# Optimization experiments

Measured on AMD Instinct MI355X. Metric: run time of the kernel, lower is better.

Reference implementation:

```python
import jax, jax.numpy as jnp
import numpy as np

B, T, DC, DS, H, V = 8, 1024, 128, 128, 512, 50000
LENGTHS = np.array([2, 4])  # dictionary word lengths for slot 0 and slot 1
LMAX = 4                    # ring-buffer size >= max word length


def setup_inputs() -> dict:
    key = jax.random.key(0)
    ks = jax.random.split(key, 12)
    s = 0.05
    return {
        "char_emb": jax.random.normal(ks[0], (B, T, DC), jnp.float32),
        "word_ids": jax.random.randint(ks[1], (B, T, 2), 0, V),
        "sense_table": jax.random.normal(ks[2], (V, DS), jnp.float32),
        "w_ih": jax.random.normal(ks[3], (DC, 3 * H), jnp.float32) * s,
        "w_hh": jax.random.normal(ks[4], (H, 3 * H), jnp.float32) * s,
        "b": jnp.zeros((3 * H,), jnp.float32),
        "aw_ih": jax.random.normal(ks[5], (DC, H), jnp.float32) * s,
        "aw_hh": jax.random.normal(ks[6], (H, H), jnp.float32) * s,
        "ab": jnp.zeros((H,), jnp.float32),
        "ww_ih": jax.random.normal(ks[7], (DS, 3 * H), jnp.float32) * s,
        "ww_hh": jax.random.normal(ks[8], (H, 3 * H), jnp.float32) * s,
        "wb": jnp.zeros((3 * H,), jnp.float32),
    }


def _forward(char_emb, word_ids, sense_table, w_ih, w_hh, b,
             aw_ih, aw_hh, ab, ww_ih, ww_hh, wb):
    H_ = w_hh.shape[0]
    T_ = char_emb.shape[1]
    lengths = jnp.asarray(LENGTHS)
    slot_idx = jnp.arange(2)

    def run_seq(x_seq, wid_seq):
        # pend: ring buffer of pending word-cell states [LMAX, 2, H]
        def step(carry, t):
            h, c, pend, pmask = carry
            x = x_seq[t]
            # --- MultiInputLSTMCell (char cell) ---
            gates = x @ w_ih + h @ w_hh + b              # [3H]
            i = jax.nn.sigmoid(gates[:H_])
            o = jax.nn.sigmoid(gates[H_:2 * H_])
            g = jnp.tanh(gates[2 * H_:])
            r = jnp.mod(t, LMAX)
            cins = pend[r]                                # [2, H] incoming word cells
            m = pmask[r].astype(x.dtype)                  # [2] validity
            alpha = jax.nn.sigmoid(x @ aw_ih + ab + cins @ aw_hh)  # [2, H]
            ea = jnp.exp(alpha) * m[:, None]
            ei = jnp.exp(i)
            denom = ei + ea.sum(0)
            c_lat = (ei * g + (ea * cins).sum(0)) / denom
            c_plain = (1.0 - i) * c + i * g               # c_num == 0 path: f = 1 - i
            c1 = jnp.where(pmask[r].any(), c_lat, c_plain)
            h1 = o * jnp.tanh(c1)
            # consume the ring slot for this timestep
            pend = pend.at[r].set(0.0)
            pmask = pmask.at[r].set(False)
            # --- WordLSTMCell for words starting at t ---
            xw = sense_table[wid_seq[t]]                  # [2, DS]
            wg = xw @ ww_ih + h1 @ ww_hh + wb             # [2, 3H]
            f = jax.nn.sigmoid(wg[:, :H_])
            iw = jax.nn.sigmoid(wg[:, H_:2 * H_])
            gw = jnp.tanh(wg[:, 2 * H_:])
            cw = f * c1 + iw * gw                         # [2, H]
            ends = t + lengths - 1
            valid = ends < T_
            wslots = jnp.mod(ends, LMAX)
            old = pend[wslots, slot_idx]
            pend = pend.at[wslots, slot_idx].set(jnp.where(valid[:, None], cw, old))
            pmask = pmask.at[wslots, slot_idx].set(valid | pmask[wslots, slot_idx])
            return (h1, c1, pend, pmask), (h1, c1)

        carry0 = (jnp.zeros((H_,), x_seq.dtype), jnp.zeros((H_,), x_seq.dtype),
                  jnp.zeros((LMAX, 2, H_), x_seq.dtype), jnp.zeros((LMAX, 2), bool))
        _, (hs, cs) = jax.lax.scan(step, carry0, jnp.arange(T_))
        return hs, cs

    hs, cs = jax.vmap(run_seq)(char_emb, word_ids)
    return jnp.stack((hs, cs))  # [2, B, T, H]


def reference(char_emb, word_ids, sense_table, w_ih, w_hh, b,
              aw_ih, aw_hh, ab, ww_ih, ww_hh, wb):
    return _forward(char_emb, word_ids, sense_table, w_ih, w_hh, b,
                    aw_ih, aw_hh, ab, ww_ih, ww_hh, wb)
```

## Files before the change

### kernel.cpp

```cpp
#include <hip/hip_runtime.h>
#include <hip/hip_bf16.h>


#define Bq 8
#define Tq 1024
#define DCq 128
#define Hq 512
#define NWG 32
#define NTHR 256

typedef unsigned long long u64;

#define HPUB_OFF  0u
#define PENDP_OFF 65536u
#define WIHT_OFF  327680u
#define WHHT_OFF  720896u
#define AWIHT_OFF 2293760u
#define AWHHT_OFF 2424832u
#define WWIHT_OFF 2949120u
#define WWHHT_OFF 3342336u

__device__ __forceinline__ float bflo(unsigned u){ return __uint_as_float(u << 16); }
__device__ __forceinline__ float bfhi(unsigned u){ return __uint_as_float(u & 0xffff0000u); }
__device__ __forceinline__ float sigm(float x){ return 1.0f / (1.0f + __expf(-x)); }

__device__ __forceinline__ void fma4(float& acc, uint2 w, float4 v){
  acc = fmaf(bflo(w.x), v.x, acc);
  acc = fmaf(bfhi(w.x), v.y, acc);
  acc = fmaf(bflo(w.y), v.z, acc);
  acc = fmaf(bfhi(w.y), v.w, acc);
}

__device__ __forceinline__ float red16(float x){
  x += __shfl_xor(x, 8, 16);
  x += __shfl_xor(x, 4, 16);
  x += __shfl_xor(x, 2, 16);
  x += __shfl_xor(x, 1, 16);
  return x;
}

__device__ __forceinline__ u64 pack64(float v, unsigned gen){
  return ((u64)gen << 32) | (u64)__float_as_uint(v);
}
__device__ __forceinline__ void pub64(u64* p, float v, unsigned gen){
  __hip_atomic_store(p, pack64(v, gen), __ATOMIC_RELAXED, __HIP_MEMORY_SCOPE_AGENT);
}
__device__ __forceinline__ u64 ld64(const u64* p){
  return __hip_atomic_load(p, __ATOMIC_RELAXED, __HIP_MEMORY_SCOPE_AGENT);
}
__device__ __forceinline__ unsigned genof(u64 v){ return (unsigned)(v >> 32); }
__device__ __forceinline__ float valof(u64 v){ return __uint_as_float((unsigned)v); }

__global__ void transpose_bf16(const float* __restrict__ src, __hip_bfloat16* __restrict__ dst,
                               int kshift, int total, int N){
  const int K = 1 << kshift;
  for (int idx = blockIdx.x * blockDim.x + threadIdx.x; idx < total;
       idx += gridDim.x * blockDim.x){
    int n = idx >> kshift;
    int k = idx & (K - 1);
    dst[idx] = __float2bfloat16(src[(size_t)k * N + n]);
  }
}

__global__ void __launch_bounds__(NTHR, 1)
lattice_main(const float* __restrict__ char_emb,
             const int*   __restrict__ word_ids,
             const float* __restrict__ sense_table,
             const float* __restrict__ bias_b,
             const float* __restrict__ bias_ab,
             const float* __restrict__ bias_wb,
             unsigned char* __restrict__ ws,
             float* __restrict__ out)
{
  const int seq  = blockIdx.x;
  const int wg   = blockIdx.y;
  const int tid  = threadIdx.x;
  const int grp  = tid >> 4;
  const int lane = tid & 15;
  const int J    = wg * 16 + grp;
  const int i0   = tid * 2, i1 = tid * 2 + 1;

  u64* hpub = (u64*)(ws + HPUB_OFF)  + (size_t)seq * 2 * Hq;
  u64* pnd  = (u64*)(ws + PENDP_OFF) + (size_t)seq * 4 * 2 * Hq;

  const uint2* w_ihT  = (const uint2*)(ws + WIHT_OFF);
  const uint2* w_hhT  = (const uint2*)(ws + WHHT_OFF);
  const uint2* aw_ihT = (const uint2*)(ws + AWIHT_OFF);
  const uint2* aw_hhT = (const uint2*)(ws + AWHHT_OFF);
  const uint2* ww_ihT = (const uint2*)(ws + WWIHT_OFF);
  const uint2* ww_hhT = (const uint2*)(ws + WWHHT_OFF);

  uint2 Rwhh_i[8], Rwhh_o[8], Rwhh_g[8], Rawhh[8];
  uint2 Rwwh_f[8], Rwwh_i[8], Rwwh_g[8];
  uint2 Rwih_i[2], Rwih_o[2], Rwih_g[2], Rawih[2];
  uint2 Rwwi_f[2], Rwwi_i[2], Rwwi_g[2];
  {
    const uint2* whh_i = w_hhT  + (size_t)(0*Hq + J) * 128;
    const uint2* whh_o = w_hhT  + (size_t)(1*Hq + J) * 128;
    const uint2* whh_g = w_hhT  + (size_t)(2*Hq + J) * 128;
    const uint2* awhh  = aw_hhT + (size_t)J * 128;
    const uint2* wwh_f = ww_hhT + (size_t)(0*Hq + J) * 128;
    const uint2* wwh_i = ww_hhT + (size_t)(1*Hq + J) * 128;
    const uint2* wwh_g = ww_hhT + (size_t)(2*Hq + J) * 128;
#pragma unroll
    for (int it = 0; it < 8; ++it){
      const int q = it * 16 + lane;
      Rwhh_i[it] = whh_i[q];  Rwhh_o[it] = whh_o[q];  Rwhh_g[it] = whh_g[q];
      Rawhh[it]  = awhh[q];
      Rwwh_f[it] = wwh_f[q];  Rwwh_i[it] = wwh_i[q];  Rwwh_g[it] = wwh_g[q];
    }
    const uint2* wih_i = w_ihT  + (size_t)(0*Hq + J) * 32;
    const uint2* wih_o = w_ihT  + (size_t)(1*Hq + J) * 32;
    const uint2* wih_g = w_ihT  + (size_t)(2*Hq + J) * 32;
    const uint2* awih  = aw_ihT + (size_t)J * 32;
    const uint2* wwi_f = ww_ihT + (size_t)(0*Hq + J) * 32;
    const uint2* wwi_i = ww_ihT + (size_t)(1*Hq + J) * 32;
    const uint2* wwi_g = ww_ihT + (size_t)(2*Hq + J) * 32;
#pragma unroll
    for (int it = 0; it < 2; ++it){
      const int q = it * 16 + lane;
      Rwih_i[it] = wih_i[q];  Rwih_o[it] = wih_o[q];  Rwih_g[it] = wih_g[q];
      Rawih[it]  = awih[q];
      Rwwi_f[it] = wwi_f[q];  Rwwi_i[it] = wwi_i[q];  Rwwi_g[it] = wwi_g[q];
    }
  }

  const float b_i  = bias_b[J], b_o = bias_b[Hq + J], b_g = bias_b[2*Hq + J];
  const float ab_J = bias_ab[J];
  const float wb_f = bias_wb[J], wb_i = bias_wb[Hq + J], wb_g = bias_wb[2*Hq + J];

  float* out_h = out + (size_t)seq * Tq * Hq;
  float* out_c = out + ((size_t)Bq + seq) * Tq * Hq;

  __shared__ __align__(16) float shH[2][Hq];
  __shared__ __align__(16) float sh_p0[Hq];
  __shared__ __align__(16) float sh_p1[Hq];
  __shared__ __align__(16) float shx[2][DCq];
  __shared__ __align__(16) float shxw0[2][DCq];
  __shared__ __align__(16) float shxw1[2][DCq];

  shH[0][i0] = 0.f; shH[0][i1] = 0.f;
  shH[1][i0] = 0.f; shH[1][i1] = 0.f;
  sh_p0[i0] = 0.f; sh_p0[i1] = 0.f;
  sh_p1[i0] = 0.f; sh_p1[i1] = 0.f;
  if (tid < DCq){
    shx[0][tid] = char_emb[((size_t)seq * Tq + 0) * DCq + tid];
  } else {
    const int k = tid - DCq;
    const int w0 = word_ids[(size_t)seq * Tq * 2 + 0];
    const int w1 = word_ids[(size_t)seq * Tq * 2 + 1];
    shxw0[0][k] = sense_table[(size_t)w0 * DCq + k];
    shxw1[0][k] = sense_table[(size_t)w1 * DCq + k];
  }
  __syncthreads();

  for (int t = 0; t < Tq; ++t){
    const int par = t & 1;
    const float* hprev = shH[par ^ 1];

    float a_i = 0.f, a_o = 0.f, a_g = 0.f, a_xa = 0.f;
#pragma unroll
    for (int it = 0; it < 8; ++it){
      const int k0 = it * 64 + lane * 4;
      float4 hv = *(const float4*)(hprev + k0);
      fma4(a_i, Rwhh_i[it], hv);
      fma4(a_o, Rwhh_o[it], hv);
      fma4(a_g, Rwhh_g[it], hv);
    }
#pragma unroll
    for (int it = 0; it < 2; ++it){
      const int k0 = it * 64 + lane * 4;
      float4 xv = *(const float4*)(shx[par] + k0);
      fma4(a_i,  Rwih_i[it], xv);
      fma4(a_o,  Rwih_o[it], xv);
      fma4(a_g,  Rwih_g[it], xv);
      fma4(a_xa, Rawih[it],  xv);
    }

    if (t >= 3){
      const u64* p0 = pnd + ((size_t)(t & 3) * 2 + 0) * Hq;
      const u64* p1 = pnd + ((size_t)(t & 3) * 2 + 1) * Hq;
      const unsigned tg0 = (unsigned)t, tg1 = (unsigned)(t - 2);
      u64 a, b, c, d;
      for (;;){
        a = ld64(p0 + i0); b = ld64(p0 + i1);
        c = ld64(p1 + i0); d = ld64(p1 + i1);
        if (genof(a) >= tg0 && genof(b) >= tg0 &&
            genof(c) >= tg1 && genof(d) >= tg1) break;
      }
      sh_p0[i0] = valof(a); sh_p0[i1] = valof(b);
      sh_p1[i0] = valof(c); sh_p1[i1] = valof(d);
    } else if (t >= 1){
      const u64* p0 = pnd + ((size_t)(t & 3) * 2 + 0) * Hq;
      const unsigned tg0 = (unsigned)t;
      u64 a, b;
      for (;;){
        a = ld64(p0 + i0); b = ld64(p0 + i1);
        if (genof(a) >= tg0 && genof(b) >= tg0) break;
      }
      sh_p0[i0] = valof(a); sh_p0[i1] = valof(b);
    }
    __syncthreads();

    float a_p0 = 0.f, a_p1 = 0.f;
#pragma unroll
    for (int it = 0; it < 8; ++it){
      const int k0 = it * 64 + lane * 4;
      float4 p0v = *(const float4*)(sh_p0 + k0);
      float4 p1v = *(const float4*)(sh_p1 + k0);
      fma4(a_p0, Rawhh[it], p0v);
      fma4(a_p1, Rawhh[it], p1v);
    }
    a_i  = red16(a_i);  a_o  = red16(a_o);  a_g  = red16(a_g);
    a_xa = red16(a_xa); a_p0 = red16(a_p0); a_p1 = red16(a_p1);

    const float gi = sigm(a_i + b_i);
    const float go = sigm(a_o + b_o);
    const float gg = tanhf(a_g + b_g);
    float c1;
    if (t == 0){
      c1 = gi * gg;
    } else {
      const float base = a_xa + ab_J;
      const float ea0 = __expf(sigm(base + a_p0));
      const float ei  = __expf(gi);
      float num = ei * gg + ea0 * sh_p0[J];
      float den = ei + ea0;
      if (t >= 3){
        const float ea1 = __expf(sigm(base + a_p1));
        num += ea1 * sh_p1[J];
        den += ea1;
      }
      c1 = num / den;
    }
    const float h1 = go * tanhf(c1);
    if (lane == 0){
      pub64(hpub + (size_t)par * Hq + J, h1, (unsigned)(t + 1));
      out_h[(size_t)t * Hq + J] = h1;
      out_c[(size_t)t * Hq + J] = c1;
    }

    {
      const int tn = (t + 1 < Tq) ? t + 1 : t;
      if (tid < DCq){
        shx[par ^ 1][tid] = char_emb[((size_t)seq * Tq + tn) * DCq + tid];
      } else {
        const int k = tid - DCq;
        const int w0 = word_ids[((size_t)seq * Tq + tn) * 2 + 0];
        const int w1 = word_ids[((size_t)seq * Tq + tn) * 2 + 1];
        shxw0[par ^ 1][k] = sense_table[(size_t)w0 * DCq + k];
        shxw1[par ^ 1][k] = sense_table[(size_t)w1 * DCq + k];
      }
      const u64* hp = hpub + (size_t)par * Hq;
      const unsigned tg = (unsigned)(t + 1);
      u64 a, b;
      for (;;){
        a = ld64(hp + i0); b = ld64(hp + i1);
        if (genof(a) >= tg && genof(b) >= tg) break;
      }
      shH[par][i0] = valof(a); shH[par][i1] = valof(b);
    }
    __syncthreads();

    float r_f = 0.f, r_i = 0.f, r_g = 0.f;
    float x_f0 = 0.f, x_i0 = 0.f, x_g0 = 0.f, x_f1 = 0.f, x_i1 = 0.f, x_g1 = 0.f;
#pragma unroll
    for (int it = 0; it < 8; ++it){
      const int k0 = it * 64 + lane * 4;
      float4 hv = *(const float4*)(shH[par] + k0);
      fma4(r_f, Rwwh_f[it], hv);
      fma4(r_i, Rwwh_i[it], hv);
      fma4(r_g, Rwwh_g[it], hv);
    }
#pragma unroll
    for (int it = 0; it < 2; ++it){
      const int k0 = it * 64 + lane * 4;
      float4 x0 = *(const float4*)(shxw0[par] + k0);
      float4 x1 = *(const float4*)(shxw1[par] + k0);
      fma4(x_f0, Rwwi_f[it], x0);  fma4(x_f1, Rwwi_f[it], x1);
      fma4(x_i0, Rwwi_i[it], x0);  fma4(x_i1, Rwwi_i[it], x1);
      fma4(x_g0, Rwwi_g[it], x0);  fma4(x_g1, Rwwi_g[it], x1);
    }
    r_f  = red16(r_f);  r_i  = red16(r_i);  r_g  = red16(r_g);
    x_f0 = red16(x_f0); x_i0 = red16(x_i0); x_g0 = red16(x_g0);
    x_f1 = red16(x_f1); x_i1 = red16(x_i1); x_g1 = red16(x_g1);

    if (lane == 0){
      const float f0  = sigm(r_f + x_f0 + wb_f);
      const float iw0 = sigm(r_i + x_i0 + wb_i);
      const float g0  = tanhf(r_g + x_g0 + wb_g);
      const float cw0 = f0 * c1 + iw0 * g0;
      const float f1  = sigm(r_f + x_f1 + wb_f);
      const float iw1 = sigm(r_i + x_i1 + wb_i);
      const float g1  = tanhf(r_g + x_g1 + wb_g);
      const float cw1 = f1 * c1 + iw1 * g1;
      pub64(pnd + ((size_t)((t + 1) & 3) * 2 + 0) * Hq + J, cw0, (unsigned)(t + 1));
      pub64(pnd + ((size_t)((t + 3) & 3) * 2 + 1) * Hq + J, cw1, (unsigned)(t + 1));
    }
  }
}

extern "C" void kernel_launch(void* const* d_in, const int* in_sizes, int n_in,
                              void* d_out, int out_size, void* d_ws, size_t ws_size,
                              hipStream_t stream){
  const float* char_emb = (const float*)d_in[0];
  const int*   word_ids = (const int*)d_in[1];
  const float* sense    = (const float*)d_in[2];
  const float* w_ih     = (const float*)d_in[3];
  const float* w_hh     = (const float*)d_in[4];
  const float* bb       = (const float*)d_in[5];
  const float* aw_ih    = (const float*)d_in[6];
  const float* aw_hh    = (const float*)d_in[7];
  const float* ab       = (const float*)d_in[8];
  const float* ww_ih    = (const float*)d_in[9];
  const float* ww_hh    = (const float*)d_in[10];
  const float* wb       = (const float*)d_in[11];
  unsigned char* ws = (unsigned char*)d_ws;
  float* out = (float*)d_out;

  hipMemsetAsync(ws, 0, WIHT_OFF, stream);

  transpose_bf16<<<512, NTHR, 0, stream>>>(w_ih,  (__hip_bfloat16*)(ws + WIHT_OFF),  7, 128*1536, 1536);
  transpose_bf16<<<512, NTHR, 0, stream>>>(w_hh,  (__hip_bfloat16*)(ws + WHHT_OFF),  9, 512*1536, 1536);
  transpose_bf16<<<512, NTHR, 0, stream>>>(aw_ih, (__hip_bfloat16*)(ws + AWIHT_OFF), 7, 128*512,  512);
  transpose_bf16<<<512, NTHR, 0, stream>>>(aw_hh, (__hip_bfloat16*)(ws + AWHHT_OFF), 9, 512*512,  512);
  transpose_bf16<<<512, NTHR, 0, stream>>>(ww_ih, (__hip_bfloat16*)(ws + WWIHT_OFF), 7, 128*1536, 1536);
  transpose_bf16<<<512, NTHR, 0, stream>>>(ww_hh, (__hip_bfloat16*)(ws + WWHHT_OFF), 9, 512*1536, 1536);

  dim3 grid(Bq, NWG);
  lattice_main<<<grid, NTHR, 0, stream>>>(char_emb, word_ids, sense, bb, ab, wb, ws, out);
}
```

Measured before the change: 5.606 ms.

## Add XCD-local fast sync path with sc0 loads and hoist word-input matvec

At startup, each workgroup reads its XCC id and publishes it, and the sequence's workgroups check whether all of them landed on the same XCD. If they did, cross-workgroup h and pending-cell exchanges use sc0-scoped global loads and stores into a separate fast buffer, falling back to the agent-scope buffer after a bounded spin. The intent is to cut the latency of the per-step cross-WG handoff by staying within the local L2 instead of going through device coherence. It also moves the word-input matvec ahead of the h spin-wait so that work overlaps the wait. The risks are extra dual stores every step and no benefit if workgroups are spread across XCDs, which is likely for the default blockIdx mapping.

```diff
diff --git a/kernel.cpp b/kernel.cpp
--- a/kernel.cpp
+++ b/kernel.cpp
@@ -8,17 +8,21 @@
 #define Hq 512
 #define NWG 32
 #define NTHR 256
+#define SPINF 64
 
 typedef unsigned long long u64;
 
-#define HPUB_OFF  0u
-#define PENDP_OFF 65536u
-#define WIHT_OFF  327680u
-#define WHHT_OFF  720896u
-#define AWIHT_OFF 2293760u
-#define AWHHT_OFF 2424832u
-#define WWIHT_OFF 2949120u
-#define WWHHT_OFF 3342336u
+#define HPUBF_OFF 0u
+#define PENDF_OFF 65536u
+#define HPUBS_OFF 327680u
+#define PENDS_OFF 393216u
+#define XCD_OFF   655360u
+#define WIHT_OFF  657408u
+#define WHHT_OFF  1050624u
+#define AWIHT_OFF 2623488u
+#define AWHHT_OFF 2754560u
+#define WWIHT_OFF 3278848u
+#define WWHHT_OFF 3672064u
 
 __device__ __forceinline__ float bflo(unsigned u){ return __uint_as_float(u << 16); }
 __device__ __forceinline__ float bfhi(unsigned u){ return __uint_as_float(u & 0xffff0000u); }
@@ -42,14 +46,38 @@
 __device__ __forceinline__ u64 pack64(float v, unsigned gen){
   return ((u64)gen << 32) | (u64)__float_as_uint(v);
 }
-__device__ __forceinline__ void pub64(u64* p, float v, unsigned gen){
-  __hip_atomic_store(p, pack64(v, gen), __ATOMIC_RELAXED, __HIP_MEMORY_SCOPE_AGENT);
+__device__ __forceinline__ void pub64(u64* p, u64 v){
+  __hip_atomic_store(p, v, __ATOMIC_RELAXED, __HIP_MEMORY_SCOPE_AGENT);
 }
 __device__ __forceinline__ u64 ld64(const u64* p){
   return __hip_atomic_load(p, __ATOMIC_RELAXED, __HIP_MEMORY_SCOPE_AGENT);
 }
 __device__ __forceinline__ unsigned genof(u64 v){ return (unsigned)(v >> 32); }
 __device__ __forceinline__ float valof(u64 v){ return __uint_as_float((unsigned)v); }
+
+__device__ __forceinline__ void st64_sc0(u64* p, u64 v){
+  asm volatile("global_store_dwordx2 %0, %1, off sc0" :: "v"(p), "v"(v) : "memory");
+}
+__device__ __forceinline__ void ld2_sc0(const u64* p0, const u64* p1, u64& a, u64& b){
+  asm volatile("global_load_dwordx2 %0, %2, off sc0\n\t"
+               "global_load_dwordx2 %1, %3, off sc0\n\t"
+               "s_waitcnt vmcnt(0)"
+               : "=&v"(a), "=&v"(b)
+               : "v"(p0), "v"(p1)
+               : "memory");
+}
+__device__ __forceinline__ void ld4_sc0(const u64* p0, const u64* p1,
+                                        const u64* p2, const u64* p3,
+                                        u64& a, u64& b, u64& c, u64& d){
+  asm volatile("global_load_dwordx2 %0, %4, off sc0\n\t"
+               "global_load_dwordx2 %1, %5, off sc0\n\t"
+               "global_load_dwordx2 %2, %6, off sc0\n\t"
+               "global_load_dwordx2 %3, %7, off sc0\n\t"
+               "s_waitcnt vmcnt(0)"
+               : "=&v"(a), "=&v"(b), "=&v"(c), "=&v"(d)
+               : "v"(p0), "v"(p1), "v"(p2), "v"(p3)
+               : "memory");
+}
 
 __global__ void transpose_bf16(const float* __restrict__ src, __hip_bfloat16* __restrict__ dst,
                                int kshift, int total, int N){
@@ -80,8 +108,10 @@
   const int J    = wg * 16 + grp;
   const int i0   = tid * 2, i1 = tid * 2 + 1;
 
-  u64* hpub = (u64*)(ws + HPUB_OFF)  + (size_t)seq * 2 * Hq;
-  u64* pnd  = (u64*)(ws + PENDP_OFF) + (size_t)seq * 4 * 2 * Hq;
+  u64* hpubf = (u64*)(ws + HPUBF_OFF) + (size_t)seq * 2 * Hq;
+  u64* hpubs = (u64*)(ws + HPUBS_OFF) + (size_t)seq * 2 * Hq;
+  u64* pndf  = (u64*)(ws + PENDF_OFF) + (size_t)seq * 4 * 2 * Hq;
+  u64* pnds  = (u64*)(ws + PENDS_OFF) + (size_t)seq * 4 * 2 * Hq;
 
   const uint2* w_ihT  = (const uint2*)(ws + WIHT_OFF);
   const uint2* w_hhT  = (const uint2*)(ws + WHHT_OFF);
@@ -138,6 +168,7 @@
   __shared__ __align__(16) float shx[2][DCq];
   __shared__ __align__(16) float shxw0[2][DCq];
   __shared__ __align__(16) float shxw1[2][DCq];
+  __shared__ int sh_fast;
 
   shH[0][i0] = 0.f; shH[0][i1] = 0.f;
   shH[1][i0] = 0.f; shH[1][i1] = 0.f;
@@ -152,7 +183,27 @@
     shxw0[0][k] = sense_table[(size_t)w0 * DCq + k];
     shxw1[0][k] = sense_table[(size_t)w1 * DCq + k];
   }
+
+  {
+    unsigned myxcc;
+    asm volatile("s_getreg_b32 %0, hwreg(HW_REG_XCC_ID)" : "=s"(myxcc));
+    u64* xcdb = (u64*)(ws + XCD_OFF) + (size_t)seq * NWG;
+    if (tid == 0){
+      pub64(&xcdb[wg], ((u64)1 << 32) | (u64)myxcc);
+    }
+    if (tid < 64){
+      bool ok = true;
+      if (tid < NWG){
+        u64 v;
+        do { v = ld64(&xcdb[tid]); } while (genof(v) == 0);
+        ok = ((unsigned)v == myxcc);
+      }
+      const unsigned long long m = __ballot(ok);
+      if (tid == 0) sh_fast = (m == ~0ull) ? 1 : 0;
+    }
+  }
   __syncthreads();
+  const bool fast = (sh_fast != 0);
 
   for (int t = 0; t < Tq; ++t){
     const int par = t & 1;
@@ -178,25 +229,56 @@
     }
 
     if (t >= 3){
-      const u64* p0 = pnd + ((size_t)(t & 3) * 2 + 0) * Hq;
-      const u64* p1 = pnd + ((size_t)(t & 3) * 2 + 1) * Hq;
       const unsigned tg0 = (unsigned)t, tg1 = (unsigned)(t - 2);
+      const u64* f0 = pndf + ((size_t)(t & 3) * 2 + 0) * Hq;
+      const u64* f1 = pndf + ((size_t)(t & 3) * 2 + 1) * Hq;
+      const u64* s0 = pnds + ((size_t)(t & 3) * 2 + 0) * Hq;
+      const u64* s1 = pnds + ((size_t)(t & 3) * 2 + 1) * Hq;
       u64 a, b, c, d;
-      for (;;){
-        a = ld64(p0 + i0); b = ld64(p0 + i1);
-        c = ld64(p1 + i0); d = ld64(p1 + i1);
-        if (genof(a) >= tg0 && genof(b) >= tg0 &&
-            genof(c) >= tg1 && genof(d) >= tg1) break;
+      bool done = false;
+      if (fast){
+        for (int s = 0; s < SPINF; ++s){
+          ld4_sc0(f0 + i0, f0 + i1, f1 + i0, f1 + i1, a, b, c, d);
+          if (genof(a) >= tg0 && genof(b) >= tg0 &&
+              genof(c) >= tg1 && genof(d) >= tg1){ done = true; break; }
+        }
+      }
+      if (!done){
+        for (;;){
+          a = ld64(s0 + i0); b = ld64(s0 + i1);
+          c = ld64(s1 + i0); d = ld64(s1 + i1);
+          if (genof(a) >= tg0 && genof(b) >= tg0 &&
+              genof(c) >= tg1 && genof(d) >= tg1) break;
+          if (fast){
+            ld4_sc0(f0 + i0, f0 + i1, f1 + i0, f1 + i1, a, b, c, d);
+            if (genof(a) >= tg0 && genof(b) >= tg0 &&
+                genof(c) >= tg1 && genof(d) >= tg1) break;
+          }
+        }
       }
       sh_p0[i0] = valof(a); sh_p0[i1] = valof(b);
       sh_p1[i0] = valof(c); sh_p1[i1] = valof(d);
     } else if (t >= 1){
-      const u64* p0 = pnd + ((size_t)(t & 3) * 2 + 0) * Hq;
       const unsigned tg0 = (unsigned)t;
+      const u64* f0 = pndf + ((size_t)(t & 3) * 2 + 0) * Hq;
+      const u64* s0 = pnds + ((size_t)(t & 3) * 2 + 0) * Hq;
       u64 a, b;
-      for (;;){
-        a = ld64(p0 + i0); b = ld64(p0 + i1);
-        if (genof(a) >= tg0 && genof(b) >= tg0) break;
+      bool done = false;
+      if (fast){
+        for (int s = 0; s < SPINF; ++s){
+          ld2_sc0(f0 + i0, f0 + i1, a, b);
+          if (genof(a) >= tg0 && genof(b) >= tg0){ done = true; break; }
+        }
+      }
+      if (!done){
+        for (;;){
+          a = ld64(s0 + i0); b = ld64(s0 + i1);
+          if (genof(a) >= tg0 && genof(b) >= tg0) break;
+          if (fast){
+            ld2_sc0(f0 + i0, f0 + i1, a, b);
+            if (genof(a) >= tg0 && genof(b) >= tg0) break;
+          }
+        }
       }
       sh_p0[i0] = valof(a); sh_p0[i1] = valof(b);
     }
@@ -235,11 +317,14 @@
     }
     const float h1 = go * tanhf(c1);
     if (lane == 0){
-      pub64(hpub + (size_t)par * Hq + J, h1, (unsigned)(t + 1));
+      const u64 pk = pack64(h1, (unsigned)(t + 1));
+      if (fast) st64_sc0(hpubf + (size_t)par * Hq + J, pk);
+      pub64(hpubs + (size_t)par * Hq + J, pk);
       out_h[(size_t)t * Hq + J] = h1;
       out_c[(size_t)t * Hq + J] = c1;
     }
 
+    float x_f0 = 0.f, x_i0 = 0.f, x_g0 = 0.f, x_f1 = 0.f, x_i1 = 0.f, x_g1 = 0.f;
     {
       const int tn = (t + 1 < Tq) ? t + 1 : t;
       if (tid < DCq){
@@ -251,19 +336,44 @@
         shxw0[par ^ 1][k] = sense_table[(size_t)w0 * DCq + k];
         shxw1[par ^ 1][k] = sense_table[(size_t)w1 * DCq + k];
       }
-      const u64* hp = hpub + (size_t)par * Hq;
+#pragma unroll
+      for (int it = 0; it < 2; ++it){
+        const int k0 = it * 64 + lane * 4;
+        float4 x0 = *(const float4*)(shxw0[par] + k0);
+        float4 x1 = *(const float4*)(shxw1[par] + k0);
+        fma4(x_f0, Rwwi_f[it], x0);  fma4(x_f1, Rwwi_f[it], x1);
+        fma4(x_i0, Rwwi_i[it], x0);  fma4(x_i1, Rwwi_i[it], x1);
+        fma4(x_g0, Rwwi_g[it], x0);  fma4(x_g1, Rwwi_g[it], x1);
+      }
+      x_f0 = red16(x_f0); x_i0 = red16(x_i0); x_g0 = red16(x_g0);
+      x_f1 = red16(x_f1); x_i1 = red16(x_i1); x_g1 = red16(x_g1);
+
       const unsigned tg = (unsigned)(t + 1);
+      const u64* hf = hpubf + (size_t)par * Hq;
+      const u64* hs = hpubs + (size_t)par * Hq;
       u64 a, b;
-      for (;;){
-        a = ld64(hp + i0); b = ld64(hp + i1);
-        if (genof(a) >= tg && genof(b) >= tg) break;
+      bool done = false;
+      if (fast){
+        for (int s = 0; s < SPINF; ++s){
+          ld2_sc0(hf + i0, hf + i1, a, b);
+          if (genof(a) >= tg && genof(b) >= tg){ done = true; break; }
+        }
+      }
+      if (!done){
+        for (;;){
+          a = ld64(hs + i0); b = ld64(hs + i1);
+          if (genof(a) >= tg && genof(b) >= tg) break;
+          if (fast){
+            ld2_sc0(hf + i0, hf + i1, a, b);
+            if (genof(a) >= tg && genof(b) >= tg) break;
+          }
+        }
       }
       shH[par][i0] = valof(a); shH[par][i1] = valof(b);
     }
     __syncthreads();
 
     float r_f = 0.f, r_i = 0.f, r_g = 0.f;
-    float x_f0 = 0.f, x_i0 = 0.f, x_g0 = 0.f, x_f1 = 0.f, x_i1 = 0.f, x_g1 = 0.f;
 #pragma unroll
     for (int it = 0; it < 8; ++it){
       const int k0 = it * 64 + lane * 4;
@@ -272,18 +382,7 @@
       fma4(r_i, Rwwh_i[it], hv);
       fma4(r_g, Rwwh_g[it], hv);
     }
-#pragma unroll
-    for (int it = 0; it < 2; ++it){
-      const int k0 = it * 64 + lane * 4;
-      float4 x0 = *(const float4*)(shxw0[par] + k0);
-      float4 x1 = *(const float4*)(shxw1[par] + k0);
-      fma4(x_f0, Rwwi_f[it], x0);  fma4(x_f1, Rwwi_f[it], x1);
-      fma4(x_i0, Rwwi_i[it], x0);  fma4(x_i1, Rwwi_i[it], x1);
-      fma4(x_g0, Rwwi_g[it], x0);  fma4(x_g1, Rwwi_g[it], x1);
-    }
-    r_f  = red16(r_f);  r_i  = red16(r_i);  r_g  = red16(r_g);
-    x_f0 = red16(x_f0); x_i0 = red16(x_i0); x_g0 = red16(x_g0);
-    x_f1 = red16(x_f1); x_i1 = red16(x_i1); x_g1 = red16(x_g1);
+    r_f = red16(r_f);  r_i = red16(r_i);  r_g = red16(r_g);
 
     if (lane == 0){
       const float f0  = sigm(r_f + x_f0 + wb_f);
@@ -294,8 +393,14 @@
       const float iw1 = sigm(r_i + x_i1 + wb_i);
       const float g1  = tanhf(r_g + x_g1 + wb_g);
       const float cw1 = f1 * c1 + iw1 * g1;
-      pub64(pnd + ((size_t)((t + 1) & 3) * 2 + 0) * Hq + J, cw0, (unsigned)(t + 1));
-      pub64(pnd + ((size_t)((t + 3) & 3) * 2 + 1) * Hq + J, cw1, (unsigned)(t + 1));
+      const u64 k0 = pack64(cw0, (unsigned)(t + 1));
+      const u64 k1 = pack64(cw1, (unsigned)(t + 1));
+      if (fast){
+        st64_sc0(pndf + ((size_t)((t + 1) & 3) * 2 + 0) * Hq + J, k0);
+        st64_sc0(pndf + ((size_t)((t + 3) & 3) * 2 + 1) * Hq + J, k1);
+      }
+      pub64(pnds + ((size_t)((t + 1) & 3) * 2 + 0) * Hq + J, k0);
+      pub64(pnds + ((size_t)((t + 3) & 3) * 2 + 1) * Hq + J, k1);
     }
   }
 }
```

New measurement: 18.15 ms. +223.8%, slower.

## Dual-publish cross-workgroup state and poll with cache-bypass vector loads

Applied to the files above, without the earlier changes.

Each published h and pending word-cell value is now written to two buffers: a plain volatile store and a relaxed agent-scope atomic store. Consumers issue an early speculative load before the matmul work and fall back to a spin loop. That loop uses inline-asm dwordx4 loads with sc0/sc1 cache bits on both copies and accepts whichever copy carries the right generation. The word-cell input matmul against sense embeddings is also moved ahead of the h-poll to overlap compute with waiting. The aim is lower cross-workgroup handoff latency per timestep, at the cost of extra stores and workspace, plus reliance on cache-coherence behaviour of sc bits.

```diff
diff --git a/kernel.cpp b/kernel.cpp
--- a/kernel.cpp
+++ b/kernel.cpp
@@ -10,15 +10,18 @@
 #define NTHR 256
 
 typedef unsigned long long u64;
-
-#define HPUB_OFF  0u
-#define PENDP_OFF 65536u
-#define WIHT_OFF  327680u
-#define WHHT_OFF  720896u
-#define AWIHT_OFF 2293760u
-#define AWHHT_OFF 2424832u
-#define WWIHT_OFF 2949120u
-#define WWHHT_OFF 3342336u
+typedef __attribute__((ext_vector_type(4))) unsigned int u32x4;
+
+#define HPUBF_OFF 0u
+#define PENDF_OFF 65536u
+#define HPUBS_OFF 327680u
+#define PENDS_OFF 393216u
+#define WIHT_OFF  657408u
+#define WHHT_OFF  1050624u
+#define AWIHT_OFF 2623488u
+#define AWHHT_OFF 2754560u
+#define WWIHT_OFF 3278848u
+#define WWHHT_OFF 3672064u
 
 __device__ __forceinline__ float bflo(unsigned u){ return __uint_as_float(u << 16); }
 __device__ __forceinline__ float bfhi(unsigned u){ return __uint_as_float(u & 0xffff0000u); }
@@ -42,14 +45,36 @@
 __device__ __forceinline__ u64 pack64(float v, unsigned gen){
   return ((u64)gen << 32) | (u64)__float_as_uint(v);
 }
-__device__ __forceinline__ void pub64(u64* p, float v, unsigned gen){
-  __hip_atomic_store(p, pack64(v, gen), __ATOMIC_RELAXED, __HIP_MEMORY_SCOPE_AGENT);
+__device__ __forceinline__ void pub64(u64* p, u64 v){
+  __hip_atomic_store(p, v, __ATOMIC_RELAXED, __HIP_MEMORY_SCOPE_AGENT);
 }
 __device__ __forceinline__ u64 ld64(const u64* p){
   return __hip_atomic_load(p, __ATOMIC_RELAXED, __HIP_MEMORY_SCOPE_AGENT);
 }
 __device__ __forceinline__ unsigned genof(u64 v){ return (unsigned)(v >> 32); }
-__device__ __forceinline__ float valof(u64 v){ return __uint_as_float((unsigned)v); }
+
+__device__ __forceinline__ void duo_load(const u64* pf, const u64* ps,
+                                         u32x4& f, u32x4& s){
+  asm volatile("global_load_dwordx4 %0, %2, off sc0\n\t"
+               "global_load_dwordx4 %1, %3, off sc1\n\t"
+               "s_waitcnt vmcnt(0)"
+               : "=&v"(f), "=&v"(s)
+               : "v"(pf), "v"(ps)
+               : "memory");
+}
+__device__ __forceinline__ void quad_load(const u64* pf0, const u64* pf1,
+                                          const u64* ps0, const u64* ps1,
+                                          u32x4& f0, u32x4& f1,
+                                          u32x4& s0, u32x4& s1){
+  asm volatile("global_load_dwordx4 %0, %4, off sc0\n\t"
+               "global_load_dwordx4 %1, %5, off sc0\n\t"
+               "global_load_dwordx4 %2, %6, off sc1\n\t"
+               "global_load_dwordx4 %3, %7, off sc1\n\t"
+               "s_waitcnt vmcnt(0)"
+               : "=&v"(f0), "=&v"(f1), "=&v"(s0), "=&v"(s1)
+               : "v"(pf0), "v"(pf1), "v"(ps0), "v"(ps1)
+               : "memory");
+}
 
 __global__ void transpose_bf16(const float* __restrict__ src, __hip_bfloat16* __restrict__ dst,
                                int kshift, int total, int N){
@@ -80,8 +105,10 @@
   const int J    = wg * 16 + grp;
   const int i0   = tid * 2, i1 = tid * 2 + 1;
 
-  u64* hpub = (u64*)(ws + HPUB_OFF)  + (size_t)seq * 2 * Hq;
-  u64* pnd  = (u64*)(ws + PENDP_OFF) + (size_t)seq * 4 * 2 * Hq;
+  u64* hpubf = (u64*)(ws + HPUBF_OFF) + (size_t)seq * 2 * Hq;
+  u64* hpubs = (u64*)(ws + HPUBS_OFF) + (size_t)seq * 2 * Hq;
+  u64* pndf  = (u64*)(ws + PENDF_OFF) + (size_t)seq * 4 * 2 * Hq;
+  u64* pnds  = (u64*)(ws + PENDS_OFF) + (size_t)seq * 4 * 2 * Hq;
 
   const uint2* w_ihT  = (const uint2*)(ws + WIHT_OFF);
   const uint2* w_hhT  = (const uint2*)(ws + WHHT_OFF);
@@ -158,6 +185,20 @@
     const int par = t & 1;
     const float* hprev = shH[par ^ 1];
 
+    const int slot = (t & 3) * 2;
+    const u64* pf0 = pndf + (size_t)(slot + 0) * Hq;
+    const u64* pf1 = pndf + (size_t)(slot + 1) * Hq;
+    const u64* ps0 = pnds + (size_t)(slot + 0) * Hq;
+    const u64* ps1 = pnds + (size_t)(slot + 1) * Hq;
+
+    u64 ea = 0, eb = 0, ec = 0, ed = 0;
+    if (t >= 3){
+      ea = ld64(ps0 + i0); eb = ld64(ps0 + i1);
+      ec = ld64(ps1 + i0); ed = ld64(ps1 + i1);
+    } else if (t >= 1){
+      ea = ld64(ps0 + i0); eb = ld64(ps0 + i1);
+    }
+
     float a_i = 0.f, a_o = 0.f, a_g = 0.f, a_xa = 0.f;
 #pragma unroll
     for (int it = 0; it < 8; ++it){
@@ -178,27 +219,43 @@
     }
 
     if (t >= 3){
-      const u64* p0 = pnd + ((size_t)(t & 3) * 2 + 0) * Hq;
-      const u64* p1 = pnd + ((size_t)(t & 3) * 2 + 1) * Hq;
       const unsigned tg0 = (unsigned)t, tg1 = (unsigned)(t - 2);
-      u64 a, b, c, d;
-      for (;;){
-        a = ld64(p0 + i0); b = ld64(p0 + i1);
-        c = ld64(p1 + i0); d = ld64(p1 + i1);
-        if (genof(a) >= tg0 && genof(b) >= tg0 &&
-            genof(c) >= tg1 && genof(d) >= tg1) break;
-      }
-      sh_p0[i0] = valof(a); sh_p0[i1] = valof(b);
-      sh_p1[i0] = valof(c); sh_p1[i1] = valof(d);
+      unsigned v00, v01, v10, v11;
+      if (genof(ea) >= tg0 && genof(eb) >= tg0 &&
+          genof(ec) >= tg1 && genof(ed) >= tg1){
+        v00 = (unsigned)ea; v01 = (unsigned)eb;
+        v10 = (unsigned)ec; v11 = (unsigned)ed;
+      } else {
+        for (;;){
+          u32x4 f0, f1, s0, s1;
+          quad_load(pf0 + i0, pf1 + i0, ps0 + i0, ps1 + i0, f0, f1, s0, s1);
+          const bool k0f = f0.y >= tg0 && f0.w >= tg0;
+          const bool k1f = f1.y >= tg1 && f1.w >= tg1;
+          const bool k0s = s0.y >= tg0 && s0.w >= tg0;
+          const bool k1s = s1.y >= tg1 && s1.w >= tg1;
+          if ((k0f || k0s) && (k1f || k1s)){
+            v00 = k0f ? f0.x : s0.x;  v01 = k0f ? f0.z : s0.z;
+            v10 = k1f ? f1.x : s1.x;  v11 = k1f ? f1.z : s1.z;
+            break;
+          }
+        }
+      }
+      sh_p0[i0] = __uint_as_float(v00); sh_p0[i1] = __uint_as_float(v01);
+      sh_p1[i0] = __uint_as_float(v10); sh_p1[i1] = __uint_as_float(v11);
     } else if (t >= 1){
-      const u64* p0 = pnd + ((size_t)(t & 3) * 2 + 0) * Hq;
       const unsigned tg0 = (unsigned)t;
-      u64 a, b;
-      for (;;){
-        a = ld64(p0 + i0); b = ld64(p0 + i1);
-        if (genof(a) >= tg0 && genof(b) >= tg0) break;
-      }
-      sh_p0[i0] = valof(a); sh_p0[i1] = valof(b);
+      unsigned v00, v01;
+      if (genof(ea) >= tg0 && genof(eb) >= tg0){
+        v00 = (unsigned)ea; v01 = (unsigned)eb;
+      } else {
+        for (;;){
+          u32x4 f, s;
+          duo_load(pf0 + i0, ps0 + i0, f, s);
+          if (f.y >= tg0 && f.w >= tg0){ v00 = f.x; v01 = f.z; break; }
+          if (s.y >= tg0 && s.w >= tg0){ v00 = s.x; v01 = s.z; break; }
+        }
+      }
+      sh_p0[i0] = __uint_as_float(v00); sh_p0[i1] = __uint_as_float(v01);
     }
     __syncthreads();
 
@@ -235,12 +292,20 @@
     }
     const float h1 = go * tanhf(c1);
     if (lane == 0){
-      pub64(hpub + (size_t)par * Hq + J, h1, (unsigned)(t + 1));
+      const u64 pk = pack64(h1, (unsigned)(t + 1));
+      *(volatile u64*)(hpubf + (size_t)par * Hq + J) = pk;
+      pub64(hpubs + (size_t)par * Hq + J, pk);
       out_h[(size_t)t * Hq + J] = h1;
       out_c[(size_t)t * Hq + J] = c1;
     }
 
+    float x_f0 = 0.f, x_i0 = 0.f, x_g0 = 0.f, x_f1 = 0.f, x_i1 = 0.f, x_g1 = 0.f;
     {
+      const u64* hf = hpubf + (size_t)par * Hq;
+      const u64* hs = hpubs + (size_t)par * Hq;
+      const unsigned tg = (unsigned)(t + 1);
+      u64 ha = ld64(hs + i0), hb = ld64(hs + i1);
+
       const int tn = (t + 1 < Tq) ? t + 1 : t;
       if (tid < DCq){
         shx[par ^ 1][tid] = char_emb[((size_t)seq * Tq + tn) * DCq + tid];
@@ -251,19 +316,34 @@
         shxw0[par ^ 1][k] = sense_table[(size_t)w0 * DCq + k];
         shxw1[par ^ 1][k] = sense_table[(size_t)w1 * DCq + k];
       }
-      const u64* hp = hpub + (size_t)par * Hq;
-      const unsigned tg = (unsigned)(t + 1);
-      u64 a, b;
-      for (;;){
-        a = ld64(hp + i0); b = ld64(hp + i1);
-        if (genof(a) >= tg && genof(b) >= tg) break;
-      }
-      shH[par][i0] = valof(a); shH[par][i1] = valof(b);
+#pragma unroll
+      for (int it = 0; it < 2; ++it){
+        const int k0 = it * 64 + lane * 4;
+        float4 x0 = *(const float4*)(shxw0[par] + k0);
+        float4 x1 = *(const float4*)(shxw1[par] + k0);
+        fma4(x_f0, Rwwi_f[it], x0);  fma4(x_f1, Rwwi_f[it], x1);
+        fma4(x_i0, Rwwi_i[it], x0);  fma4(x_i1, Rwwi_i[it], x1);
+        fma4(x_g0, Rwwi_g[it], x0);  fma4(x_g1, Rwwi_g[it], x1);
+      }
+      x_f0 = red16(x_f0); x_i0 = red16(x_i0); x_g0 = red16(x_g0);
+      x_f1 = red16(x_f1); x_i1 = red16(x_i1); x_g1 = red16(x_g1);
+
+      unsigned va, vb;
+      if (genof(ha) >= tg && genof(hb) >= tg){
+        va = (unsigned)ha; vb = (unsigned)hb;
+      } else {
+        for (;;){
+          u32x4 f, s;
+          duo_load(hf + i0, hs + i0, f, s);
+          if (f.y >= tg && f.w >= tg){ va = f.x; vb = f.z; break; }
+          if (s.y >= tg && s.w >= tg){ va = s.x; vb = s.z; break; }
+        }
+      }
+      shH[par][i0] = __uint_as_float(va); shH[par][i1] = __uint_as_float(vb);
     }
     __syncthreads();
 
     float r_f = 0.f, r_i = 0.f, r_g = 0.f;
-    float x_f0 = 0.f, x_i0 = 0.f, x_g0 = 0.f, x_f1 = 0.f, x_i1 = 0.f, x_g1 = 0.f;
 #pragma unroll
     for (int it = 0; it < 8; ++it){
       const int k0 = it * 64 + lane * 4;
@@ -272,18 +352,7 @@
       fma4(r_i, Rwwh_i[it], hv);
       fma4(r_g, Rwwh_g[it], hv);
     }
-#pragma unroll
-    for (int it = 0; it < 2; ++it){
-      const int k0 = it * 64 + lane * 4;
-      float4 x0 = *(const float4*)(shxw0[par] + k0);
-      float4 x1 = *(const float4*)(shxw1[par] + k0);
-      fma4(x_f0, Rwwi_f[it], x0);  fma4(x_f1, Rwwi_f[it], x1);
-      fma4(x_i0, Rwwi_i[it], x0);  fma4(x_i1, Rwwi_i[it], x1);
-      fma4(x_g0, Rwwi_g[it], x0);  fma4(x_g1, Rwwi_g[it], x1);
-    }
-    r_f  = red16(r_f);  r_i  = red16(r_i);  r_g  = red16(r_g);
-    x_f0 = red16(x_f0); x_i0 = red16(x_i0); x_g0 = red16(x_g0);
-    x_f1 = red16(x_f1); x_i1 = red16(x_i1); x_g1 = red16(x_g1);
+    r_f = red16(r_f);  r_i = red16(r_i);  r_g = red16(r_g);
 
     if (lane == 0){
       const float f0  = sigm(r_f + x_f0 + wb_f);
@@ -294,8 +363,14 @@
       const float iw1 = sigm(r_i + x_i1 + wb_i);
       const float g1  = tanhf(r_g + x_g1 + wb_g);
       const float cw1 = f1 * c1 + iw1 * g1;
-      pub64(pnd + ((size_t)((t + 1) & 3) * 2 + 0) * Hq + J, cw0, (unsigned)(t + 1));
-      pub64(pnd + ((size_t)((t + 3) & 3) * 2 + 1) * Hq + J, cw1, (unsigned)(t + 1));
+      const u64 pk0 = pack64(cw0, (unsigned)(t + 1));
+      const u64 pk1 = pack64(cw1, (unsigned)(t + 1));
+      const size_t o0 = ((size_t)((t + 1) & 3) * 2 + 0) * Hq + J;
+      const size_t o1 = ((size_t)((t + 3) & 3) * 2 + 1) * Hq + J;
+      *(volatile u64*)(pndf + o0) = pk0;
+      *(volatile u64*)(pndf + o1) = pk1;
+      pub64(pnds + o0, pk0);
+      pub64(pnds + o1, pk1);
     }
   }
 }
```

After: 8.245 ms. 1.47x slower.

## Spread hidden columns over twice as many workgroups and prefetch sync flags

Applied to the files above, without the earlier changes.

Each workgroup now owns 8 hidden columns instead of 16, with 32 lanes per column, so the grid doubles to 512 workgroups and per-thread register weights halve. Polling loads for the pending word-cell and hidden-state flags are issued before the matvec work, so their latency overlaps compute and a spin loop runs only if the first read is stale. The word-input projection is moved ahead of the hidden-state wait. The cost is more workgroups in each cross-workgroup barrier, more global flag traffic, and longer shuffle reductions.

```diff
diff --git a/kernel.cpp b/kernel.cpp
--- a/kernel.cpp
+++ b/kernel.cpp
@@ -6,19 +6,20 @@
 #define Tq 1024
 #define DCq 128
 #define Hq 512
-#define NWG 32
+#define NWGY 64
+#define COLS 8
 #define NTHR 256
 
 typedef unsigned long long u64;
 
-#define HPUB_OFF  0u
-#define PENDP_OFF 65536u
-#define WIHT_OFF  327680u
-#define WHHT_OFF  720896u
-#define AWIHT_OFF 2293760u
-#define AWHHT_OFF 2424832u
-#define WWIHT_OFF 2949120u
-#define WWHHT_OFF 3342336u
+#define HPUB_OFF 0u
+#define PEND_OFF 65536u
+#define WIHT_OFF  657408u
+#define WHHT_OFF  1050624u
+#define AWIHT_OFF 2623488u
+#define AWHHT_OFF 2754560u
+#define WWIHT_OFF 3278848u
+#define WWHHT_OFF 3672064u
 
 __device__ __forceinline__ float bflo(unsigned u){ return __uint_as_float(u << 16); }
 __device__ __forceinline__ float bfhi(unsigned u){ return __uint_as_float(u & 0xffff0000u); }
@@ -31,19 +32,20 @@
   acc = fmaf(bfhi(w.y), v.w, acc);
 }
 
-__device__ __forceinline__ float red16(float x){
-  x += __shfl_xor(x, 8, 16);
-  x += __shfl_xor(x, 4, 16);
-  x += __shfl_xor(x, 2, 16);
-  x += __shfl_xor(x, 1, 16);
+__device__ __forceinline__ float red32(float x){
+  x += __shfl_xor(x, 16, 32);
+  x += __shfl_xor(x, 8, 32);
+  x += __shfl_xor(x, 4, 32);
+  x += __shfl_xor(x, 2, 32);
+  x += __shfl_xor(x, 1, 32);
   return x;
 }
 
 __device__ __forceinline__ u64 pack64(float v, unsigned gen){
   return ((u64)gen << 32) | (u64)__float_as_uint(v);
 }
-__device__ __forceinline__ void pub64(u64* p, float v, unsigned gen){
-  __hip_atomic_store(p, pack64(v, gen), __ATOMIC_RELAXED, __HIP_MEMORY_SCOPE_AGENT);
+__device__ __forceinline__ void pub64(u64* p, u64 v){
+  __hip_atomic_store(p, v, __ATOMIC_RELAXED, __HIP_MEMORY_SCOPE_AGENT);
 }
 __device__ __forceinline__ u64 ld64(const u64* p){
   return __hip_atomic_load(p, __ATOMIC_RELAXED, __HIP_MEMORY_SCOPE_AGENT);
@@ -62,7 +64,7 @@
   }
 }
 
-__global__ void __launch_bounds__(NTHR, 1)
+__global__ void __launch_bounds__(NTHR, 2)
 lattice_main(const float* __restrict__ char_emb,
              const int*   __restrict__ word_ids,
              const float* __restrict__ sense_table,
@@ -75,26 +77,21 @@
   const int seq  = blockIdx.x;
   const int wg   = blockIdx.y;
   const int tid  = threadIdx.x;
-  const int grp  = tid >> 4;
-  const int lane = tid & 15;
-  const int J    = wg * 16 + grp;
+  const int grp  = tid >> 5;
+  const int lane = tid & 31;
+  const int J    = wg * COLS + grp;
   const int i0   = tid * 2, i1 = tid * 2 + 1;
 
-  u64* hpub = (u64*)(ws + HPUB_OFF)  + (size_t)seq * 2 * Hq;
-  u64* pnd  = (u64*)(ws + PENDP_OFF) + (size_t)seq * 4 * 2 * Hq;
-
-  const uint2* w_ihT  = (const uint2*)(ws + WIHT_OFF);
-  const uint2* w_hhT  = (const uint2*)(ws + WHHT_OFF);
-  const uint2* aw_ihT = (const uint2*)(ws + AWIHT_OFF);
-  const uint2* aw_hhT = (const uint2*)(ws + AWHHT_OFF);
-  const uint2* ww_ihT = (const uint2*)(ws + WWIHT_OFF);
-  const uint2* ww_hhT = (const uint2*)(ws + WWHHT_OFF);
-
-  uint2 Rwhh_i[8], Rwhh_o[8], Rwhh_g[8], Rawhh[8];
-  uint2 Rwwh_f[8], Rwwh_i[8], Rwwh_g[8];
-  uint2 Rwih_i[2], Rwih_o[2], Rwih_g[2], Rawih[2];
-  uint2 Rwwi_f[2], Rwwi_i[2], Rwwi_g[2];
+  u64* hpub = (u64*)(ws + HPUB_OFF) + (size_t)seq * 2 * Hq;
+  u64* pnd  = (u64*)(ws + PEND_OFF) + (size_t)seq * 4 * 2 * Hq;
+
+  uint2 Rwhh_i[4], Rwhh_o[4], Rwhh_g[4], Rawhh[4];
+  uint2 Rwwh_f[4], Rwwh_i[4], Rwwh_g[4];
+  uint2 Rwih_i, Rwih_o, Rwih_g, Rawih, Rwwi_f, Rwwi_i, Rwwi_g;
   {
+    const uint2* w_hhT  = (const uint2*)(ws + WHHT_OFF);
+    const uint2* aw_hhT = (const uint2*)(ws + AWHHT_OFF);
+    const uint2* ww_hhT = (const uint2*)(ws + WWHHT_OFF);
     const uint2* whh_i = w_hhT  + (size_t)(0*Hq + J) * 128;
     const uint2* whh_o = w_hhT  + (size_t)(1*Hq + J) * 128;
     const uint2* whh_g = w_hhT  + (size_t)(2*Hq + J) * 128;
@@ -103,26 +100,22 @@
     const uint2* wwh_i = ww_hhT + (size_t)(1*Hq + J) * 128;
     const uint2* wwh_g = ww_hhT + (size_t)(2*Hq + J) * 128;
 #pragma unroll
-    for (int it = 0; it < 8; ++it){
-      const int q = it * 16 + lane;
+    for (int it = 0; it < 4; ++it){
+      const int q = it * 32 + lane;
       Rwhh_i[it] = whh_i[q];  Rwhh_o[it] = whh_o[q];  Rwhh_g[it] = whh_g[q];
       Rawhh[it]  = awhh[q];
       Rwwh_f[it] = wwh_f[q];  Rwwh_i[it] = wwh_i[q];  Rwwh_g[it] = wwh_g[q];
     }
-    const uint2* wih_i = w_ihT  + (size_t)(0*Hq + J) * 32;
-    const uint2* wih_o = w_ihT  + (size_t)(1*Hq + J) * 32;
-    const uint2* wih_g = w_ihT  + (size_t)(2*Hq + J) * 32;
-    const uint2* awih  = aw_ihT + (size_t)J * 32;
-    const uint2* wwi_f = ww_ihT + (size_t)(0*Hq + J) * 32;
-    const uint2* wwi_i = ww_ihT + (size_t)(1*Hq + J) * 32;
-    const uint2* wwi_g = ww_ihT + (size_t)(2*Hq + J) * 32;
-#pragma unroll
-    for (int it = 0; it < 2; ++it){
-      const int q = it * 16 + lane;
-      Rwih_i[it] = wih_i[q];  Rwih_o[it] = wih_o[q];  Rwih_g[it] = wih_g[q];
-      Rawih[it]  = awih[q];
-      Rwwi_f[it] = wwi_f[q];  Rwwi_i[it] = wwi_i[q];  Rwwi_g[it] = wwi_g[q];
-    }
+    const uint2* w_ihT  = (const uint2*)(ws + WIHT_OFF);
+    const uint2* aw_ihT = (const uint2*)(ws + AWIHT_OFF);
+    const uint2* ww_ihT = (const uint2*)(ws + WWIHT_OFF);
+    Rwih_i = (w_ihT  + (size_t)(0*Hq + J) * 32)[lane];
+    Rwih_o = (w_ihT  + (size_t)(1*Hq + J) * 32)[lane];
+    Rwih_g = (w_ihT  + (size_t)(2*Hq + J) * 32)[lane];
+    Rawih  = (aw_ihT + (size_t)J * 32)[lane];
+    Rwwi_f = (ww_ihT + (size_t)(0*Hq + J) * 32)[lane];
+    Rwwi_i = (ww_ihT + (size_t)(1*Hq + J) * 32)[lane];
+    Rwwi_g = (ww_ihT + (size_t)(2*Hq + J) * 32)[lane];
   }
 
   const float b_i  = bias_b[J], b_o = bias_b[Hq + J], b_g = bias_b[2*Hq + J];
@@ -158,61 +151,70 @@
     const int par = t & 1;
     const float* hprev = shH[par ^ 1];
 
+    const u64* p0 = pnd + ((size_t)(t & 3) * 2 + 0) * Hq;
+    const u64* p1 = pnd + ((size_t)(t & 3) * 2 + 1) * Hq;
+    u64 ea = 0, eb = 0, ec = 0, ed = 0;
+    if (t >= 3){
+      ea = ld64(p0 + i0); eb = ld64(p0 + i1);
+      ec = ld64(p1 + i0); ed = ld64(p1 + i1);
+    } else if (t >= 1){
+      ea = ld64(p0 + i0); eb = ld64(p0 + i1);
+    }
+
     float a_i = 0.f, a_o = 0.f, a_g = 0.f, a_xa = 0.f;
 #pragma unroll
-    for (int it = 0; it < 8; ++it){
-      const int k0 = it * 64 + lane * 4;
+    for (int it = 0; it < 4; ++it){
+      const int k0 = it * 128 + lane * 4;
       float4 hv = *(const float4*)(hprev + k0);
       fma4(a_i, Rwhh_i[it], hv);
       fma4(a_o, Rwhh_o[it], hv);
       fma4(a_g, Rwhh_g[it], hv);
     }
-#pragma unroll
-    for (int it = 0; it < 2; ++it){
-      const int k0 = it * 64 + lane * 4;
+    {
+      const int k0 = lane * 4;
       float4 xv = *(const float4*)(shx[par] + k0);
-      fma4(a_i,  Rwih_i[it], xv);
-      fma4(a_o,  Rwih_o[it], xv);
-      fma4(a_g,  Rwih_g[it], xv);
-      fma4(a_xa, Rawih[it],  xv);
+      fma4(a_i,  Rwih_i, xv);
+      fma4(a_o,  Rwih_o, xv);
+      fma4(a_g,  Rwih_g, xv);
+      fma4(a_xa, Rawih,  xv);
     }
 
     if (t >= 3){
-      const u64* p0 = pnd + ((size_t)(t & 3) * 2 + 0) * Hq;
-      const u64* p1 = pnd + ((size_t)(t & 3) * 2 + 1) * Hq;
       const unsigned tg0 = (unsigned)t, tg1 = (unsigned)(t - 2);
-      u64 a, b, c, d;
-      for (;;){
-        a = ld64(p0 + i0); b = ld64(p0 + i1);
-        c = ld64(p1 + i0); d = ld64(p1 + i1);
-        if (genof(a) >= tg0 && genof(b) >= tg0 &&
-            genof(c) >= tg1 && genof(d) >= tg1) break;
-      }
-      sh_p0[i0] = valof(a); sh_p0[i1] = valof(b);
-      sh_p1[i0] = valof(c); sh_p1[i1] = valof(d);
+      if (!(genof(ea) >= tg0 && genof(eb) >= tg0 &&
+            genof(ec) >= tg1 && genof(ed) >= tg1)){
+        for (;;){
+          ea = ld64(p0 + i0); eb = ld64(p0 + i1);
+          ec = ld64(p1 + i0); ed = ld64(p1 + i1);
+          if (genof(ea) >= tg0 && genof(eb) >= tg0 &&
+              genof(ec) >= tg1 && genof(ed) >= tg1) break;
+        }
+      }
+      sh_p0[i0] = valof(ea); sh_p0[i1] = valof(eb);
+      sh_p1[i0] = valof(ec); sh_p1[i1] = valof(ed);
     } else if (t >= 1){
-      const u64* p0 = pnd + ((size_t)(t & 3) * 2 + 0) * Hq;
       const unsigned tg0 = (unsigned)t;
-      u64 a, b;
-      for (;;){
-        a = ld64(p0 + i0); b = ld64(p0 + i1);
-        if (genof(a) >= tg0 && genof(b) >= tg0) break;
-      }
-      sh_p0[i0] = valof(a); sh_p0[i1] = valof(b);
+      if (!(genof(ea) >= tg0 && genof(eb) >= tg0)){
+        for (;;){
+          ea = ld64(p0 + i0); eb = ld64(p0 + i1);
+          if (genof(ea) >= tg0 && genof(eb) >= tg0) break;
+        }
+      }
+      sh_p0[i0] = valof(ea); sh_p0[i1] = valof(eb);
     }
     __syncthreads();
 
     float a_p0 = 0.f, a_p1 = 0.f;
 #pragma unroll
-    for (int it = 0; it < 8; ++it){
-      const int k0 = it * 64 + lane * 4;
+    for (int it = 0; it < 4; ++it){
+      const int k0 = it * 128 + lane * 4;
       float4 p0v = *(const float4*)(sh_p0 + k0);
       float4 p1v = *(const float4*)(sh_p1 + k0);
       fma4(a_p0, Rawhh[it], p0v);
       fma4(a_p1, Rawhh[it], p1v);
     }
-    a_i  = red16(a_i);  a_o  = red16(a_o);  a_g  = red16(a_g);
-    a_xa = red16(a_xa); a_p0 = red16(a_p0); a_p1 = red16(a_p1);
+    a_i  = red32(a_i);  a_o  = red32(a_o);  a_g  = red32(a_g);
+    a_xa = red32(a_xa); a_p0 = red32(a_p0); a_p1 = red32(a_p1);
 
     const float gi = sigm(a_i + b_i);
     const float go = sigm(a_o + b_o);
@@ -235,12 +237,17 @@
     }
     const float h1 = go * tanhf(c1);
     if (lane == 0){
-      pub64(hpub + (size_t)par * Hq + J, h1, (unsigned)(t + 1));
+      pub64(hpub + (size_t)par * Hq + J, pack64(h1, (unsigned)(t + 1)));
       out_h[(size_t)t * Hq + J] = h1;
       out_c[(size_t)t * Hq + J] = c1;
     }
 
+    float x_f0 = 0.f, x_i0 = 0.f, x_g0 = 0.f, x_f1 = 0.f, x_i1 = 0.f, x_g1 = 0.f;
     {
+      const u64* hp = hpub + (size_t)par * Hq;
+      const unsigned tg = (unsigned)(t + 1);
+      u64 ha = ld64(hp + i0), hb = ld64(hp + i1);
+
       const int tn = (t + 1 < Tq) ? t + 1 : t;
       if (tid < DCq){
         shx[par ^ 1][tid] = char_emb[((size_t)seq * Tq + tn) * DCq + tid];
@@ -251,51 +258,51 @@
         shxw0[par ^ 1][k] = sense_table[(size_t)w0 * DCq + k];
         shxw1[par ^ 1][k] = sense_table[(size_t)w1 * DCq + k];
       }
-      const u64* hp = hpub + (size_t)par * Hq;
-      const unsigned tg = (unsigned)(t + 1);
-      u64 a, b;
-      for (;;){
-        a = ld64(hp + i0); b = ld64(hp + i1);
-        if (genof(a) >= tg && genof(b) >= tg) break;
-      }
-      shH[par][i0] = valof(a); shH[par][i1] = valof(b);
+      {
+        const int k0 = lane * 4;
+        float4 x0 = *(const float4*)(shxw0[par] + k0);
+        float4 x1 = *(const float4*)(shxw1[par] + k0);
+        fma4(x_f0, Rwwi_f, x0);  fma4(x_f1, Rwwi_f, x1);
+        fma4(x_i0, Rwwi_i, x0);  fma4(x_i1, Rwwi_i, x1);
+        fma4(x_g0, Rwwi_g, x0);  fma4(x_g1, Rwwi_g, x1);
+      }
+      x_f0 = red32(x_f0); x_i0 = red32(x_i0); x_g0 = red32(x_g0);
+      x_f1 = red32(x_f1); x_i1 = red32(x_i1); x_g1 = red32(x_g1);
+
+      if (!(genof(ha) >= tg && genof(hb) >= tg)){
+        for (;;){
+          ha = ld64(hp + i0); hb = ld64(hp + i1);
+          if (genof(ha) >= tg && genof(hb) >= tg) break;
+        }
+      }
+      shH[par][i0] = valof(ha); shH[par][i1] = valof(hb);
     }
     __syncthreads();
 
     float r_f = 0.f, r_i = 0.f, r_g = 0.f;
-    float x_f0 = 0.f, x_i0 = 0.f, x_g0 = 0.f, x_f1 = 0.f, x_i1 = 0.f, x_g1 = 0.f;
 #pragma unroll
-    for (int it = 0; it < 8; ++it){
-      const int k0 = it * 64 + lane * 4;
+    for (int it = 0; it < 4; ++it){
+      const int k0 = it * 128 + lane * 4;
       float4 hv = *(const float4*)(shH[par] + k0);
       fma4(r_f, Rwwh_f[it], hv);
       fma4(r_i, Rwwh_i[it], hv);
       fma4(r_g, Rwwh_g[it], hv);
     }
-#pragma unroll
-    for (int it = 0; it < 2; ++it){
-      const int k0 = it * 64 + lane * 4;
-      float4 x0 = *(const float4*)(shxw0[par] + k0);
-      float4 x1 = *(const float4*)(shxw1[par] + k0);
-      fma4(x_f0, Rwwi_f[it], x0);  fma4(x_f1, Rwwi_f[it], x1);
-      fma4(x_i0, Rwwi_i[it], x0);  fma4(x_i1, Rwwi_i[it], x1);
-      fma4(x_g0, Rwwi_g[it], x0);  fma4(x_g1, Rwwi_g[it], x1);
-    }
-    r_f  = red16(r_f);  r_i  = red16(r_i);  r_g  = red16(r_g);
-    x_f0 = red16(x_f0); x_i0 = red16(x_i0); x_g0 = red16(x_g0);
-    x_f1 = red16(x_f1); x_i1 = red16(x_i1); x_g1 = red16(x_g1);
+    r_f = red32(r_f);  r_i = red32(r_i);  r_g = red32(r_g);
 
     if (lane == 0){
       const float f0  = sigm(r_f + x_f0 + wb_f);
       const float iw0 = sigm(r_i + x_i0 + wb_i);
       const float g0  = tanhf(r_g + x_g0 + wb_g);
       const float cw0 = f0 * c1 + iw0 * g0;
+      pub64(pnd + ((size_t)((t + 1) & 3) * 2 + 0) * Hq + J,
+            pack64(cw0, (unsigned)(t + 1)));
       const float f1  = sigm(r_f + x_f1 + wb_f);
       const float iw1 = sigm(r_i + x_i1 + wb_i);
       const float g1  = tanhf(r_g + x_g1 + wb_g);
       const float cw1 = f1 * c1 + iw1 * g1;
-      pub64(pnd + ((size_t)((t + 1) & 3) * 2 + 0) * Hq + J, cw0, (unsigned)(t + 1));
-      pub64(pnd + ((size_t)((t + 3) & 3) * 2 + 1) * Hq + J, cw1, (unsigned)(t + 1));
+      pub64(pnd + ((size_t)((t + 3) & 3) * 2 + 1) * Hq + J,
+            pack64(cw1, (unsigned)(t + 1)));
     }
   }
 }
@@ -327,6 +334,6 @@
   transpose_bf16<<<512, NTHR, 0, stream>>>(ww_ih, (__hip_bfloat16*)(ws + WWIHT_OFF), 7, 128*1536, 1536);
   transpose_bf16<<<512, NTHR, 0, stream>>>(ww_hh, (__hip_bfloat16*)(ws + WWHHT_OFF), 9, 512*1536, 1536);
 
-  dim3 grid(Bq, NWG);
+  dim3 grid(Bq, NWGY);
   lattice_main<<<grid, NTHR, 0, stream>>>(char_emb, word_ids, sense, bb, ab, wb, ws, out);
 }
```

New measurement: 9.678 ms. +72.6%, slower.
